# Kernel optimization log

Hardware: AMD Instinct MI355X
Metric: run time of the kernel (lower is better)

The kernel has to match this reference:

```python
import jax, jax.numpy as jnp
import numpy as np

EPS = 1e-12  # torch F.normalize default eps


def _l2norm(t, axis=-1):
    n = jnp.sqrt(jnp.sum(t * t, axis=axis, keepdims=True))
    return t / jnp.maximum(n, EPS)


def setup_inputs() -> dict:
    key = jax.random.key(0)
    ks = jax.random.split(key, 5)
    B, N, C, H = 8, 4096, 1024, 16
    x = jax.random.normal(ks[0], (B, N, C), dtype=jnp.float32)
    # nn.Linear(dim, 3*dim, bias=False): weight [3C, C]; we store transposed [C, 3C]
    w_qkv = jax.random.normal(ks[1], (C, 3 * C), dtype=jnp.float32) * (1.0 / np.sqrt(C))
    temperature = jnp.ones((H, 1, 1), dtype=jnp.float32)
    w_proj = jax.random.normal(ks[2], (C, C), dtype=jnp.float32) * (1.0 / np.sqrt(C))
    b_proj = jax.random.normal(ks[3], (C,), dtype=jnp.float32) * 0.01
    return {"x": x, "w_qkv": w_qkv, "temperature": temperature,
            "w_proj": w_proj, "b_proj": b_proj}


def reference(x, w_qkv, temperature, w_proj, b_proj):
    B, N, C = x.shape
    H = temperature.shape[0]
    dh = C // H
    # qkv: [B, N, 3C] -> [B, N, 3, H, dh] -> q/k/v each [B, H, dh, N]
    qkv = (x @ w_qkv).reshape(B, N, 3, H, dh).transpose(2, 0, 3, 4, 1)
    q, k, v = qkv[0], qkv[1], qkv[2]
    # L2-normalize over token axis (last dim)
    q = _l2norm(q)
    k = _l2norm(k)
    # channel-channel attention: [B, H, dh, dh]
    attn = jnp.einsum("bhdn,bhen->bhde", q, k) * temperature  # temp broadcasts [H,1,1]
    attn = jax.nn.softmax(attn, axis=-1)
    # weighted sum over channels: [B, H, dh, N] -> [B, N, C]
    out = jnp.einsum("bhde,bhen->bhdn", attn, v).transpose(0, 3, 1, 2).reshape(B, N, C)
    return out @ w_proj + b_proj
```

## Files before the change

kernel.cpp:

```cpp
#include <hip/hip_runtime.h>
#include <cstdint>

typedef unsigned short u16;
typedef unsigned int u32;
typedef __attribute__((ext_vector_type(8))) short bf16x8;
typedef __attribute__((ext_vector_type(4))) float f32x4;

typedef const u32 __attribute__((address_space(1)))* gp_t;
typedef u32 __attribute__((address_space(3)))* lp_t;

__device__ __forceinline__ u16 f2bf(float f) {
    union { float f; u32 u; } v; v.f = f;
    u32 r = v.u + 0x7FFFu + ((v.u >> 16) & 1u);
    return (u16)(r >> 16);
}
__device__ __forceinline__ float bf2f(u16 h) {
    union { u32 u; float f; } v; v.u = ((u32)h) << 16;
    return v.f;
}

__global__ __launch_bounds__(256) void k_pack2(const float* __restrict__ x,
                                               u16* __restrict__ xt, u16* __restrict__ xc) {
    __shared__ u16 tb[64][72];
    const int blk = blockIdx.x;
    const int tt = blk >> 4, ct = blk & 15;
    const long tok0 = (long)tt * 64;
    const int ch0 = ct * 64;
    const int tid = threadIdx.x;
    const int row = tid >> 2, cq = tid & 3;
#pragma unroll
    for (int jj = 0; jj < 4; ++jj) {
        const float4 v = *(const float4*)(x + (tok0 + row) * 1024 + ch0 + cq * 16 + jj * 4);
        tb[row][cq * 16 + jj * 4 + 0] = f2bf(v.x);
        tb[row][cq * 16 + jj * 4 + 1] = f2bf(v.y);
        tb[row][cq * 16 + jj * 4 + 2] = f2bf(v.z);
        tb[row][cq * 16 + jj * 4 + 3] = f2bf(v.w);
    }
    __syncthreads();
#pragma unroll
    for (int s = 0; s < 2; ++s) {
        const int c = s * 256 + tid;
        const int r2 = c >> 3, col8 = c & 7;
        *(uint4*)(xt + (tok0 + r2) * 1024 + ch0 + col8 * 8) = *(const uint4*)(&tb[r2][col8 * 8]);
    }
    const int b = (int)(tok0 >> 12);
    const int nin = (int)(tok0 & 4095);
#pragma unroll
    for (int s = 0; s < 2; ++s) {
        const int c = s * 256 + tid;
        const int crow = c >> 3, t8 = c & 7;
        u16 u[8];
#pragma unroll
        for (int k = 0; k < 8; ++k) u[k] = tb[t8 * 8 + k][crow];
        *(uint4*)(xc + ((long)b * 1024 + ch0 + crow) * 4096 + nin + t8 * 8) = *(const uint4*)u;
    }
}

__global__ void k_transpose_w(const float* __restrict__ src, u16* __restrict__ dst, int ncols) {
    __shared__ float t[64][65];
    int ntn = ncols >> 6;
    int kb = (blockIdx.x / ntn) * 64;
    int nb = (blockIdx.x % ntn) * 64;
    for (int i = threadIdx.x; i < 4096; i += 256) {
        int r = i >> 6, c = i & 63;
        t[r][c] = src[(long)(kb + r) * ncols + nb + c];
    }
    __syncthreads();
    for (int i = threadIdx.x; i < 4096; i += 256) {
        int r = i >> 6, c = i & 63;
        dst[(long)(nb + r) * 1024 + kb + c] = f2bf(t[c][r]);
    }
}

__global__ __launch_bounds__(256) void k_pack_wv(const float* __restrict__ wqkv, u16* __restrict__ wvb) {
    const int idx = blockIdx.x * 256 + threadIdx.x;
    const int cin = idx >> 7, e0 = (idx & 127) * 8;
    const float4 v1 = *(const float4*)(wqkv + (long)cin * 3072 + 2048 + e0);
    const float4 v2 = *(const float4*)(wqkv + (long)cin * 3072 + 2048 + e0 + 4);
    u16 u[8];
    u[0] = f2bf(v1.x); u[1] = f2bf(v1.y); u[2] = f2bf(v1.z); u[3] = f2bf(v1.w);
    u[4] = f2bf(v2.x); u[5] = f2bf(v2.y); u[6] = f2bf(v2.z); u[7] = f2bf(v2.w);
    *(uint4*)(wvb + (long)cin * 1024 + e0) = *(const uint4*)u;
}

__global__ __launch_bounds__(256) void k_g128p(
    const u16* __restrict__ xc, float* __restrict__ Sp)
{
    __shared__ u16 sm[8192];

    const int tid = threadIdx.x;
    const int wid = tid >> 6, lane = tid & 63;
    const int wr = wid >> 1, wc = wid & 1;
    const int fr = lane & 15, sl = lane >> 4;

    const int nwg = gridDim.x;
    const int logical = (blockIdx.x & 7) * (nwg >> 3) + (blockIdx.x >> 3);
    const int kseg = logical & 3;
    const int bt = logical >> 2;
    const int b = bt / 36;
    int t = bt % 36;
    int i0 = 0;
    while (t >= 8 - i0) { t -= 8 - i0; ++i0; }
    const int j0 = i0 + t;
    const int m0 = i0 * 128, n0 = j0 * 128;

    const u16* base = xc + (long)b * 4194304 + kseg * 1024;

    const int srow = lane >> 2;
    const int sslot = lane & 3;

    f32x4 acc[4][4];
#pragma unroll
    for (int i = 0; i < 4; ++i)
#pragma unroll
        for (int j = 0; j < 4; ++j) acc[i][j] = (f32x4){0.f, 0.f, 0.f, 0.f};

    for (int kt = 0; kt < 1024; kt += 32) {
        __syncthreads();
#pragma unroll
        for (int i = 0; i < 2; ++i) {
            const int row = wid * 32 + i * 16 + srow;
            const int swz = (sslot ^ ((row >> 1) & 3)) << 3;
            const u16* ga = base + (long)(m0 + row) * 4096 + kt + swz;
            const u16* gb = base + (long)(n0 + row) * 4096 + kt + swz;
            __builtin_amdgcn_global_load_lds((gp_t)ga, (lp_t)(sm + (wid * 2 + i) * 512), 16, 0, 0);
            __builtin_amdgcn_global_load_lds((gp_t)gb, (lp_t)(sm + 4096 + (wid * 2 + i) * 512), 16, 0, 0);
        }
        __syncthreads();
        bf16x8 af[4], bfr[4];
#pragma unroll
        for (int mi = 0; mi < 4; ++mi) {
            const int row = wr * 64 + mi * 16 + fr;
            af[mi] = *(const bf16x8*)(sm + row * 32 + ((sl ^ ((row >> 1) & 3)) << 3));
        }
#pragma unroll
        for (int ni = 0; ni < 4; ++ni) {
            const int row = wc * 64 + ni * 16 + fr;
            bfr[ni] = *(const bf16x8*)(sm + 4096 + row * 32 + ((sl ^ ((row >> 1) & 3)) << 3));
        }
#pragma unroll
        for (int mi = 0; mi < 4; ++mi)
#pragma unroll
            for (int ni = 0; ni < 4; ++ni)
                acc[mi][ni] = __builtin_amdgcn_mfma_f32_16x16x32_bf16(af[mi], bfr[ni], acc[mi][ni], 0, 0, 0);
    }

    float* gp = Sp + (long)logical * 16384;
#pragma unroll
    for (int mi = 0; mi < 4; ++mi)
#pragma unroll
        for (int ni = 0; ni < 4; ++ni)
#pragma unroll
            for (int rr = 0; rr < 4; ++rr)
                gp[(wr * 64 + mi * 16 + sl * 4 + rr) * 128 + wc * 64 + ni * 16 + fr] = acc[mi][ni][rr];
}

__global__ __launch_bounds__(256) void k_sred(const float* __restrict__ Sp, u16* __restrict__ S)
{
    __shared__ u16 lC[128 * 136];
    __shared__ u16 lCT[128 * 136];

    const int tid = threadIdx.x;
    const int nwg = gridDim.x;
    const int logical = (blockIdx.x & 7) * (nwg >> 3) + (blockIdx.x >> 3);
    const int b = logical / 36;
    int t = logical % 36;
    int i0 = 0;
    while (t >= 8 - i0) { t -= 8 - i0; ++i0; }
    const int j0 = i0 + t;
    const int m0 = i0 * 128, n0 = j0 * 128;

    const float* p = Sp + (long)logical * 65536;
    for (int i = tid; i < 16384; i += 256) {
        const float s = p[i] + p[i + 16384] + p[i + 32768] + p[i + 49152];
        const u16 v = f2bf(s);
        const int r_ = i >> 7, c_ = i & 127;
        lC[r_ * 136 + c_] = v;
        lCT[c_ * 136 + r_] = v;
    }
    __syncthreads();
    const int tk = tid >> 1, half = tid & 1;
    {
        u16* dp = S + (long)b * 1048576 + (long)(m0 + tk) * 1024 + n0 + half * 64;
        const u16* sp1 = lC + tk * 136 + half * 64;
#pragma unroll
        for (int i = 0; i < 8; ++i) ((uint4*)dp)[i] = ((const uint4*)sp1)[i];
    }
    if (i0 != j0) {
        u16* dp = S + (long)b * 1048576 + (long)(n0 + tk) * 1024 + m0 + half * 64;
        const u16* sp2 = lCT + tk * 136 + half * 64;
#pragma unroll
        for (int i = 0; i < 8; ++i) ((uint4*)dp)[i] = ((const uint4*)sp2)[i];
    }
}

__global__ __launch_bounds__(256) void k_g128(
    const u16* __restrict__ A, long Ab, const u16* __restrict__ Bt, long Bs,
    u16* __restrict__ C, long Cb, int K, int MT, int NT)
{
    __shared__ u16 sm[8192];
    __shared__ u16 lC[128 * 136];

    const int tid = threadIdx.x;
    const int wid = tid >> 6, lane = tid & 63;
    const int wr = wid >> 1, wc = wid & 1;
    const int fr = lane & 15, sl = lane >> 4;

    const int nwg = gridDim.x;
    const int logical = (blockIdx.x & 7) * (nwg >> 3) + (blockIdx.x >> 3);

    const int b = logical / (MT * NT);
    const int r = logical % (MT * NT);
    const int i0 = r / NT, j0 = r % NT;
    const int m0 = i0 * 128, n0 = j0 * 128;
    const u16* Abp = A + (long)b * Ab;
    const u16* Bbp = Bt + (long)b * Bs;
    u16* Cbp = C + (long)b * Cb;

    const int srow = lane >> 2;
    const int sslot = lane & 3;

    f32x4 acc[4][4];
#pragma unroll
    for (int i = 0; i < 4; ++i)
#pragma unroll
        for (int j = 0; j < 4; ++j) acc[i][j] = (f32x4){0.f, 0.f, 0.f, 0.f};

    for (int kt = 0; kt < K; kt += 32) {
        __syncthreads();
#pragma unroll
        for (int i = 0; i < 2; ++i) {
            const int row = wid * 32 + i * 16 + srow;
            const int swz = (sslot ^ ((row >> 1) & 3)) << 3;
            const u16* ga = Abp + (long)(m0 + row) * K + kt + swz;
            const u16* gb = Bbp + (long)(n0 + row) * K + kt + swz;
            __builtin_amdgcn_global_load_lds((gp_t)ga, (lp_t)(sm + (wid * 2 + i) * 512), 16, 0, 0);
            __builtin_amdgcn_global_load_lds((gp_t)gb, (lp_t)(sm + 4096 + (wid * 2 + i) * 512), 16, 0, 0);
        }
        __syncthreads();
        bf16x8 af[4], bfr[4];
#pragma unroll
        for (int mi = 0; mi < 4; ++mi) {
            const int row = wr * 64 + mi * 16 + fr;
            af[mi] = *(const bf16x8*)(sm + row * 32 + ((sl ^ ((row >> 1) & 3)) << 3));
        }
#pragma unroll
        for (int ni = 0; ni < 4; ++ni) {
            const int row = wc * 64 + ni * 16 + fr;
            bfr[ni] = *(const bf16x8*)(sm + 4096 + row * 32 + ((sl ^ ((row >> 1) & 3)) << 3));
        }
#pragma unroll
        for (int mi = 0; mi < 4; ++mi)
#pragma unroll
            for (int ni = 0; ni < 4; ++ni)
                acc[mi][ni] = __builtin_amdgcn_mfma_f32_16x16x32_bf16(af[mi], bfr[ni], acc[mi][ni], 0, 0, 0);
    }
    __syncthreads();

#pragma unroll
    for (int mi = 0; mi < 4; ++mi)
#pragma unroll
        for (int ni = 0; ni < 4; ++ni) {
            const int ch = wc * 64 + ni * 16 + fr;
            const int tk = wr * 64 + mi * 16 + sl * 4;
#pragma unroll
            for (int rr = 0; rr < 4; ++rr)
                lC[(tk + rr) * 136 + ch] = f2bf(acc[mi][ni][rr]);
        }
    __syncthreads();
    {
        const int tk = tid >> 1, half = tid & 1;
        const u16* sp = lC + tk * 136 + half * 64;
        u16* dp = Cbp + (long)(m0 + tk) * 1024 + n0 + half * 64;
#pragma unroll
        for (int i = 0; i < 8; ++i) ((uint4*)dp)[i] = ((const uint4*)sp)[i];
    }
}

template<int EPI>
__global__ __launch_bounds__(512, 2) void k_gemm256(
    const u16* __restrict__ A, long Ab, const u16* __restrict__ Bt, long Bs,
    int MT, int NT,
    u16* __restrict__ cB, float* __restrict__ cF, long Cb, const float* __restrict__ bias)
{
    __shared__ uint4 smem4[8704];
    u16* sm = (u16*)smem4;

    const int tid = threadIdx.x;
    const int wid = tid >> 6, lane = tid & 63;
    const int wr = wid >> 2, wc = wid & 3;
    const int fr = lane & 15, sl = lane >> 4;

    const int nwg = gridDim.x;
    const int logical = (blockIdx.x & 7) * (nwg >> 3) + (blockIdx.x >> 3);
    const int b = logical / (MT * NT);
    const int rem = logical % (MT * NT);
    const int mt = rem / NT, nt = rem % NT;
    const long m0 = (long)mt * 256;
    const int n0 = nt * 256;

    const int srow = wid * 32 + (lane >> 2);
    const int kswz = (((lane & 3) ^ ((srow >> 1) & 3)) << 3);
    const u16* gA = A + (long)b * Ab + (m0 + srow) * 1024L + kswz;
    const u16* gB = Bt + (long)b * Bs + ((long)n0 + srow) * 1024L + kswz;
    const int ldst = wid * 1024;

    const int fxor = ((sl ^ ((fr >> 1) & 3)) << 3);
    const int aBase = (wr * 128 + fr) * 32 + fxor;
    const int bBase = 32768 + (wc * 64 + fr) * 32 + fxor;

    f32x4 acc[8][4];
#pragma unroll
    for (int i = 0; i < 8; ++i)
#pragma unroll
        for (int j = 0; j < 4; ++j) acc[i][j] = (f32x4){0.f, 0.f, 0.f, 0.f};

#define STAGE_A(d, kh, ts) do { \
    const u16* g_ = gA + (ts) * 64 + (kh) * 32; \
    u16* l_ = sm + (d) * 16384 + (kh) * 8192 + ldst; \
    __builtin_amdgcn_global_load_lds((gp_t)g_, (lp_t)l_, 16, 0, 0); \
    __builtin_amdgcn_global_load_lds((gp_t)(g_ + 16 * 1024), (lp_t)(l_ + 512), 16, 0, 0); \
} while (0)
#define STAGE_B(d, kh, ts) do { \
    const u16* g_ = gB + (ts) * 64 + (kh) * 32; \
    u16* l_ = sm + 32768 + (d) * 16384 + (kh) * 8192 + ldst; \
    __builtin_amdgcn_global_load_lds((gp_t)g_, (lp_t)l_, 16, 0, 0); \
    __builtin_amdgcn_global_load_lds((gp_t)(g_ + 16 * 1024), (lp_t)(l_ + 512), 16, 0, 0); \
} while (0)

    STAGE_A(0, 0, 0); STAGE_B(0, 0, 0);
    STAGE_A(0, 1, 0); STAGE_B(0, 1, 0);
    STAGE_A(1, 0, 1); STAGE_B(1, 0, 1);
    asm volatile("s_waitcnt vmcnt(8)" ::: "memory");
    __builtin_amdgcn_s_barrier();

    bf16x8 afX[4], afY[4], bfX[4], bfY[4];
#pragma unroll
    for (int ni = 0; ni < 4; ++ni) bfX[ni] = *(const bf16x8*)(sm + bBase + ni * 512);
#pragma unroll
    for (int mi = 0; mi < 4; ++mi) afX[mi] = *(const bf16x8*)(sm + aBase + mi * 512);

#pragma unroll 2
    for (int T = 0; T < 16; ++T) {
        const int d = T & 1;
        const int t1 = (T + 1 < 16) ? T + 1 : 15;
        const int t2 = (T + 2 < 16) ? T + 2 : 15;
        const int base = d * 16384;
        const int nbase = (d ^ 1) * 16384;

#pragma unroll
        for (int mi = 0; mi < 4; ++mi)
            afY[mi] = *(const bf16x8*)(sm + aBase + (4 + mi) * 512 + base);
        STAGE_A(d ^ 1, 1, t1);
        asm volatile("s_waitcnt vmcnt(6)" ::: "memory");
        __builtin_amdgcn_s_barrier();
        __builtin_amdgcn_s_setprio(1);
#pragma unroll
        for (int mi = 0; mi < 4; ++mi)
#pragma unroll
            for (int ni = 0; ni < 4; ++ni)
                acc[mi][ni] = __builtin_amdgcn_mfma_f32_16x16x32_bf16(afX[mi], bfX[ni], acc[mi][ni], 0, 0, 0);
        __builtin_amdgcn_s_setprio(0);
        __builtin_amdgcn_s_barrier();

#pragma unroll
        for (int ni = 0; ni < 4; ++ni)
            bfY[ni] = *(const bf16x8*)(sm + bBase + ni * 512 + base + 8192);
#pragma unroll
        for (int mi = 0; mi < 4; ++mi)
            afX[mi] = *(const bf16x8*)(sm + aBase + mi * 512 + base + 8192);
        STAGE_B(d ^ 1, 1, t1);
        __builtin_amdgcn_s_barrier();
        __builtin_amdgcn_s_setprio(1);
#pragma unroll
        for (int mi = 0; mi < 4; ++mi)
#pragma unroll
            for (int ni = 0; ni < 4; ++ni)
                acc[mi + 4][ni] = __builtin_amdgcn_mfma_f32_16x16x32_bf16(afY[mi], bfX[ni], acc[mi + 4][ni], 0, 0, 0);
        __builtin_amdgcn_s_setprio(0);
        __builtin_amdgcn_s_barrier();

#pragma unroll
        for (int mi = 0; mi < 4; ++mi)
            afY[mi] = *(const bf16x8*)(sm + aBase + (4 + mi) * 512 + base + 8192);
        STAGE_A(d, 0, t2);
        asm volatile("s_waitcnt vmcnt(6)" ::: "memory");
        __builtin_amdgcn_s_barrier();
        __builtin_amdgcn_s_setprio(1);
#pragma unroll
        for (int mi = 0; mi < 4; ++mi)
#pragma unroll
            for (int ni = 0; ni < 4; ++ni)
                acc[mi][ni] = __builtin_amdgcn_mfma_f32_16x16x32_bf16(afX[mi], bfY[ni], acc[mi][ni], 0, 0, 0);
        __builtin_amdgcn_s_setprio(0);
        __builtin_amdgcn_s_barrier();

#pragma unroll
        for (int ni = 0; ni < 4; ++ni)
            bfX[ni] = *(const bf16x8*)(sm + bBase + ni * 512 + nbase);
#pragma unroll
        for (int mi = 0; mi < 4; ++mi)
            afX[mi] = *(const bf16x8*)(sm + aBase + mi * 512 + nbase);
        STAGE_B(d, 0, t2);
        __builtin_amdgcn_s_barrier();
        __builtin_amdgcn_s_setprio(1);
#pragma unroll
        for (int mi = 0; mi < 4; ++mi)
#pragma unroll
            for (int ni = 0; ni < 4; ++ni)
                acc[mi + 4][ni] = __builtin_amdgcn_mfma_f32_16x16x32_bf16(afY[mi], bfY[ni], acc[mi + 4][ni], 0, 0, 0);
        __builtin_amdgcn_s_setprio(0);
        __builtin_amdgcn_s_barrier();
    }
#undef STAGE_A
#undef STAGE_B
    asm volatile("s_waitcnt vmcnt(0)" ::: "memory");
    __syncthreads();

    if (EPI == 0) {
        u16* cbase = cB + (long)b * Cb;
        u16* piece = sm + wid * 8704;
#pragma unroll
        for (int mi = 0; mi < 8; ++mi)
#pragma unroll
            for (int ni = 0; ni < 4; ++ni) {
                const int ch = ni * 16 + fr;
                const int tk = mi * 16 + sl * 4;
#pragma unroll
                for (int rr = 0; rr < 4; ++rr)
                    piece[(tk + rr) * 68 + ch] = f2bf(acc[mi][ni][rr]);
            }
        __syncthreads();
#pragma unroll
        for (int i = 0; i < 32; ++i) {
            const int chunk = i * 512 + tid;
            const int row = chunk >> 4, c8 = chunk & 15;
            const int p = row >> 7, tk = row & 127;
            const int wrp = p >> 2, wcp = p & 3;
            const uint2 v = *(const uint2*)(sm + p * 8704 + tk * 68 + c8 * 4);
            *(uint2*)(cbase + (m0 + wrp * 128 + tk) * 1024L + n0 + wcp * 64 + c8 * 4) = v;
        }
    } else {
        float* cbase = cF + (long)b * Cb;
        float bi[4];
#pragma unroll
        for (int ni = 0; ni < 4; ++ni) bi[ni] = bias[n0 + wc * 64 + ni * 16 + fr];
#pragma unroll
        for (int pass = 0; pass < 2; ++pass) {
            float* pieceF = (float*)smem4 + wid * 4352;
            if (pass) __syncthreads();
#pragma unroll
            for (int mi2 = 0; mi2 < 4; ++mi2) {
                const int mi = pass * 4 + mi2;
#pragma unroll
                for (int ni = 0; ni < 4; ++ni) {
                    const int ch = ni * 16 + fr;
                    const int tk = mi2 * 16 + sl * 4;
#pragma unroll
                    for (int rr = 0; rr < 4; ++rr)
                        pieceF[(tk + rr) * 68 + ch] = acc[mi][ni][rr] + bi[ni];
                }
            }
            __syncthreads();
#pragma unroll
            for (int i = 0; i < 16; ++i) {
                const int chunk = i * 512 + tid;
                const int row = chunk >> 4, c4 = chunk & 15;
                const int p = row >> 6, tk = row & 63;
                const int wrp = p >> 2, wcp = p & 3;
                const float4 v = *(const float4*)((float*)smem4 + p * 4352 + tk * 68 + c4 * 4);
                *(float4*)(cbase + (m0 + wrp * 128 + pass * 64 + tk) * 1024L + n0 + wcp * 64 + c4 * 4) = v;
            }
        }
    }
}

__global__ __launch_bounds__(256) void k_gram2p(
    const u16* __restrict__ wqT, const u16* __restrict__ Ut,
    float* __restrict__ g2p, float* __restrict__ sq2p)
{
    __shared__ u16 lQ[64 * 256];
    __shared__ u16 lK[64 * 256];

    const int blk = blockIdx.x;
    const int seg = blk & 3, bh = blk >> 2;
    const int b = bh >> 4, h = bh & 15;
    const int tid = threadIdx.x;
    const int wid = tid >> 6, lane = tid & 63;

    {
        const int r2 = lane >> 5, slot = lane & 31;
        const int rbase = wid * 16;
#pragma unroll
        for (int i = 0; i < 8; ++i) {
            const int r = rbase + i * 2 + r2;
            const int col = seg * 256 + ((slot ^ (r & 7)) << 3);
            const u16* gq = wqT + (long)(h * 64 + r) * 1024 + col;
            const u16* gk = Ut + ((long)b * 2048 + 1024 + h * 64 + r) * 1024 + col;
            __builtin_amdgcn_global_load_lds((gp_t)gq, (lp_t)(lQ + (rbase + i * 2) * 256), 16, 0, 0);
            __builtin_amdgcn_global_load_lds((gp_t)gk, (lp_t)(lK + (rbase + i * 2) * 256), 16, 0, 0);
        }
    }
    __syncthreads();

    {
        const int row = tid >> 1, half = tid & 1;
        const int j = (row < 64) ? (h * 64 + row) : (1024 + h * 64 + (row - 64));
        const u16* pa = wqT + (long)j * 1024 + seg * 256 + half * 128;
        const u16* pb = Ut + ((long)b * 2048 + j) * 1024 + seg * 256 + half * 128;
        float s = 0.f;
#pragma unroll 4
        for (int i = 0; i < 16; ++i) {
            const uint4 a = *(const uint4*)(pa + i * 8);
            const uint4 bv = *(const uint4*)(pb + i * 8);
            s += bf2f((u16)(a.x & 0xFFFF)) * bf2f((u16)(bv.x & 0xFFFF));
            s += bf2f((u16)(a.x >> 16))    * bf2f((u16)(bv.x >> 16));
            s += bf2f((u16)(a.y & 0xFFFF)) * bf2f((u16)(bv.y & 0xFFFF));
            s += bf2f((u16)(a.y >> 16))    * bf2f((u16)(bv.y >> 16));
            s += bf2f((u16)(a.z & 0xFFFF)) * bf2f((u16)(bv.z & 0xFFFF));
            s += bf2f((u16)(a.z >> 16))    * bf2f((u16)(bv.z >> 16));
            s += bf2f((u16)(a.w & 0xFFFF)) * bf2f((u16)(bv.w & 0xFFFF));
            s += bf2f((u16)(a.w >> 16))    * bf2f((u16)(bv.w >> 16));
        }
        s += __shfl_xor(s, 1);
        if (half == 0) sq2p[(long)blk * 128 + row] = s;
    }

    const int fr = lane & 15, sl = lane >> 4;
    f32x4 acc[4];
#pragma unroll
    for (int i = 0; i < 4; ++i) acc[i] = (f32x4){0.f, 0.f, 0.f, 0.f};
#pragma unroll
    for (int ks = 0; ks < 8; ++ks) {
        const int ra = wid * 16 + fr;
        const bf16x8 a = *(const bf16x8*)(lQ + ra * 256 + (((ks * 4 + sl) ^ (ra & 7)) << 3));
#pragma unroll
        for (int ni = 0; ni < 4; ++ni) {
            const int rb = ni * 16 + fr;
            const bf16x8 bb = *(const bf16x8*)(lK + rb * 256 + (((ks * 4 + sl) ^ (rb & 7)) << 3));
            acc[ni] = __builtin_amdgcn_mfma_f32_16x16x32_bf16(a, bb, acc[ni], 0, 0, 0);
        }
    }
    float* gp = g2p + (long)blk * 4096;
#pragma unroll
    for (int ni = 0; ni < 4; ++ni)
#pragma unroll
        for (int rr = 0; rr < 4; ++rr)
            gp[(wid * 16 + sl * 4 + rr) * 64 + ni * 16 + fr] = acc[ni][rr];
}

__global__ __launch_bounds__(256) void k_smax2(
    const float* __restrict__ g2p, const float* __restrict__ sq2p,
    const float* __restrict__ temperature, u16* __restrict__ attn_g)
{
    const int row = blockIdx.x * 4 + (threadIdx.x >> 6);
    const int e = threadIdx.x & 63;
    const int bh = row >> 6, d = row & 63;
    const int h = bh & 15;
    float raw = 0.f, sqq = 0.f, sqk = 0.f;
    const float* gp = g2p + (long)bh * 16384 + d * 64 + e;
    const float* sp = sq2p + (long)bh * 512;
#pragma unroll
    for (int s = 0; s < 4; ++s) {
        raw += gp[s * 4096];
        sqq += sp[s * 128 + d];
        sqk += sp[s * 128 + 64 + e];
    }
    const float rq = 1.f / fmaxf(sqrtf(sqq), 1e-12f);
    const float rk = 1.f / fmaxf(sqrtf(sqk), 1e-12f);
    const float v = raw * rq * rk * temperature[h];
    float mx = v;
#pragma unroll
    for (int o = 32; o; o >>= 1) mx = fmaxf(mx, __shfl_xor(mx, o));
    const float p = __expf(v - mx);
    float sum = p;
#pragma unroll
    for (int o = 32; o; o >>= 1) sum += __shfl_xor(sum, o);
    attn_g[(long)row * 64 + e] = f2bf(p / sum);
}

__global__ __launch_bounds__(256) void k_wmix(
    const u16* __restrict__ attn_g, const u16* __restrict__ wpT, u16* __restrict__ wmix)
{
    __shared__ u16 lA[64 * 72];
    __shared__ u16 lB[256 * 64];

    const int blk = blockIdx.x;
    const int nseg = blk & 3, bh = blk >> 2;
    const int b = bh >> 4, h = bh & 15;
    const int tid = threadIdx.x;
    const int wid = tid >> 6, lane = tid & 63;
    const int fr = lane & 15, sl = lane >> 4;

#pragma unroll
    for (int i = 0; i < 8; ++i) {
        const int cc = wid * 8 + i;
        const int row = cc * 8 + (lane >> 3);
        const int slot = lane & 7;
        const u16* g = wpT + (long)(nseg * 256 + row) * 1024 + h * 64 + ((slot ^ (row & 7)) << 3);
        __builtin_amdgcn_global_load_lds((gp_t)g, (lp_t)(lB + cc * 512), 16, 0, 0);
    }
    {
        const u16* src = attn_g + (long)bh * 4096;
        for (int i = tid; i < 4096; i += 256) {
            const int d = i >> 6, e = i & 63;
            lA[e * 72 + d] = src[i];
        }
    }
    __syncthreads();

    f32x4 acc[4][4];
#pragma unroll
    for (int i = 0; i < 4; ++i)
#pragma unroll
        for (int j = 0; j < 4; ++j) acc[i][j] = (f32x4){0.f, 0.f, 0.f, 0.f};

#pragma unroll
    for (int ks = 0; ks < 2; ++ks) {
        bf16x8 a[4], bb[4];
#pragma unroll
        for (int mi = 0; mi < 4; ++mi)
            a[mi] = *(const bf16x8*)(lA + (mi * 16 + fr) * 72 + ks * 32 + sl * 8);
#pragma unroll
        for (int ni = 0; ni < 4; ++ni) {
            const int rb = wid * 64 + ni * 16 + fr;
            bb[ni] = *(const bf16x8*)(lB + rb * 64 + (((ks * 4 + sl) ^ (rb & 7)) << 3));
        }
#pragma unroll
        for (int mi = 0; mi < 4; ++mi)
#pragma unroll
            for (int ni = 0; ni < 4; ++ni)
                acc[mi][ni] = __builtin_amdgcn_mfma_f32_16x16x32_bf16(a[mi], bb[ni], acc[mi][ni], 0, 0, 0);
    }

    u16* dst = wmix + ((long)b << 20);
#pragma unroll
    for (int mi = 0; mi < 4; ++mi)
#pragma unroll
        for (int ni = 0; ni < 4; ++ni) {
            const int cout = nseg * 256 + wid * 64 + ni * 16 + fr;
            const int e0 = mi * 16 + sl * 4;
            ushort4 w;
            w.x = f2bf(acc[mi][ni][0]); w.y = f2bf(acc[mi][ni][1]);
            w.z = f2bf(acc[mi][ni][2]); w.w = f2bf(acc[mi][ni][3]);
            *(ushort4*)(dst + (long)cout * 1024 + h * 64 + e0) = w;
        }
}

extern "C" void kernel_launch(void* const* d_in, const int* in_sizes, int n_in,
                              void* d_out, int out_size, void* d_ws, size_t ws_size,
                              hipStream_t stream) {
    const float* x = (const float*)d_in[0];
    const float* w_qkv = (const float*)d_in[1];
    const float* temperature = (const float*)d_in[2];
    const float* w_proj = (const float*)d_in[3];
    const float* b_proj = (const float*)d_in[4];
    float* out = (float*)d_out;
    char* ws = (char*)d_ws;

    u16* wqT    = (u16*)(ws);
    u16* wpT    = (u16*)(ws + 6291456);
    u16* wvb    = (u16*)(ws + 8388608);
    u16* xt     = (u16*)(ws + 10485760);
    u16* xc     = (u16*)(ws + 77594624);
    u16* S      = (u16*)(ws + 144703488);
    float* Sp   = (float*)(ws + 161480704);
    u16* Ut     = (u16*)(ws + 161480704);
    float* g2p  = (float*)(ws + 195035136);
    float* sq2p = (float*)(ws + 203423744);
    u16* attn_g = (u16*)(ws + 203685888);
    u16* wmix   = (u16*)(ws + 204734464);
    u16* wfinT  = (u16*)(ws + 221511680);

    k_pack2<<<8192, 256, 0, stream>>>(x, xt, xc);
    k_transpose_w<<<768, 256, 0, stream>>>(w_qkv, wqT, 3072);
    k_transpose_w<<<256, 256, 0, stream>>>(w_proj, wpT, 1024);
    k_pack_wv<<<512, 256, 0, stream>>>(w_qkv, wvb);
    k_g128p<<<1152, 256, 0, stream>>>(xc, Sp);
    k_sred<<<288, 256, 0, stream>>>(Sp, S);
    k_gemm256<0><<<256, 512, 0, stream>>>(wqT, 0L, S, 1048576L, 8, 4, Ut, nullptr, 2097152L, nullptr);
    k_gram2p<<<512, 256, 0, stream>>>(wqT, Ut, g2p, sq2p);
    k_smax2<<<2048, 256, 0, stream>>>(g2p, sq2p, temperature, attn_g);
    k_wmix<<<512, 256, 0, stream>>>(attn_g, wpT, wmix);
    k_g128<<<512, 256, 0, stream>>>(wmix, 1048576L, wvb, 0L, wfinT, 1048576L, 1024, 8, 8);
    k_gemm256<1><<<512, 512, 0, stream>>>(xt, 4194304L, wfinT, 1048576L, 16, 4, nullptr, out, 4194304L, b_proj);
}
```

Before: 345.6 us.

## Merge weight prep kernels, fuse softmax into wmix, replace 256-tile GEMMs with 128-tile

Three weight-preparation kernels become one launch, and the softmax kernel is folded into the attention-weight mixing kernel so the bf16 attention matrix never round-trips through global memory. The heavily pipelined 256x256 GEMM kernel is removed. Its two uses now go to the simpler single-buffered 128x128 GEMM kernels, including a new float-output variant with a bias epilogue. This cuts launches and intermediate traffic, but gives up the deep double-buffered, priority-scheduled main loop in the largest GEMM, which may lower MFMA throughput.

```diff
diff --git a/kernel.cpp b/kernel.cpp
--- a/kernel.cpp
+++ b/kernel.cpp
@@ -56,31 +56,39 @@
     }
 }
 
-__global__ void k_transpose_w(const float* __restrict__ src, u16* __restrict__ dst, int ncols) {
+__global__ __launch_bounds__(256) void k_prep(
+    const float* __restrict__ wqkv, const float* __restrict__ wproj,
+    u16* __restrict__ wqT, u16* __restrict__ wpT, u16* __restrict__ wvb)
+{
     __shared__ float t[64][65];
-    int ntn = ncols >> 6;
-    int kb = (blockIdx.x / ntn) * 64;
-    int nb = (blockIdx.x % ntn) * 64;
-    for (int i = threadIdx.x; i < 4096; i += 256) {
-        int r = i >> 6, c = i & 63;
-        t[r][c] = src[(long)(kb + r) * ncols + nb + c];
-    }
-    __syncthreads();
-    for (int i = threadIdx.x; i < 4096; i += 256) {
-        int r = i >> 6, c = i & 63;
-        dst[(long)(nb + r) * 1024 + kb + c] = f2bf(t[c][r]);
-    }
-}
-
-__global__ __launch_bounds__(256) void k_pack_wv(const float* __restrict__ wqkv, u16* __restrict__ wvb) {
-    const int idx = blockIdx.x * 256 + threadIdx.x;
-    const int cin = idx >> 7, e0 = (idx & 127) * 8;
-    const float4 v1 = *(const float4*)(wqkv + (long)cin * 3072 + 2048 + e0);
-    const float4 v2 = *(const float4*)(wqkv + (long)cin * 3072 + 2048 + e0 + 4);
-    u16 u[8];
-    u[0] = f2bf(v1.x); u[1] = f2bf(v1.y); u[2] = f2bf(v1.z); u[3] = f2bf(v1.w);
-    u[4] = f2bf(v2.x); u[5] = f2bf(v2.y); u[6] = f2bf(v2.z); u[7] = f2bf(v2.w);
-    *(uint4*)(wvb + (long)cin * 1024 + e0) = *(const uint4*)u;
+    const int blk = blockIdx.x;
+    const int tid = threadIdx.x;
+    if (blk < 1024) {
+        const float* src; u16* dst; int ncols, lb;
+        if (blk < 768) { src = wqkv; dst = wqT; ncols = 3072; lb = blk; }
+        else           { src = wproj; dst = wpT; ncols = 1024; lb = blk - 768; }
+        const int ntn = ncols >> 6;
+        const int kb = (lb / ntn) * 64;
+        const int nb = (lb % ntn) * 64;
+        for (int i = tid; i < 4096; i += 256) {
+            int r = i >> 6, c = i & 63;
+            t[r][c] = src[(long)(kb + r) * ncols + nb + c];
+        }
+        __syncthreads();
+        for (int i = tid; i < 4096; i += 256) {
+            int r = i >> 6, c = i & 63;
+            dst[(long)(nb + r) * 1024 + kb + c] = f2bf(t[c][r]);
+        }
+    } else {
+        const int idx = (blk - 1024) * 256 + tid;
+        const int cin = idx >> 7, e0 = (idx & 127) * 8;
+        const float4 v1 = *(const float4*)(wqkv + (long)cin * 3072 + 2048 + e0);
+        const float4 v2 = *(const float4*)(wqkv + (long)cin * 3072 + 2048 + e0 + 4);
+        u16 u[8];
+        u[0] = f2bf(v1.x); u[1] = f2bf(v1.y); u[2] = f2bf(v1.z); u[3] = f2bf(v1.w);
+        u[4] = f2bf(v2.x); u[5] = f2bf(v2.y); u[6] = f2bf(v2.z); u[7] = f2bf(v2.w);
+        *(uint4*)(wvb + (long)cin * 1024 + e0) = *(const uint4*)u;
+    }
 }
 
 __global__ __launch_bounds__(256) void k_g128p(
@@ -277,200 +285,95 @@
     }
 }
 
-template<int EPI>
-__global__ __launch_bounds__(512, 2) void k_gemm256(
+__global__ __launch_bounds__(256) void k_g128f(
     const u16* __restrict__ A, long Ab, const u16* __restrict__ Bt, long Bs,
-    int MT, int NT,
-    u16* __restrict__ cB, float* __restrict__ cF, long Cb, const float* __restrict__ bias)
-{
-    __shared__ uint4 smem4[8704];
-    u16* sm = (u16*)smem4;
+    float* __restrict__ C, long Cb, int K, int MT, int NT, const float* __restrict__ bias)
+{
+    __shared__ u16 sm[8192];
+    __shared__ float lCf[4 * 2176];
 
     const int tid = threadIdx.x;
     const int wid = tid >> 6, lane = tid & 63;
-    const int wr = wid >> 2, wc = wid & 3;
+    const int wr = wid >> 1, wc = wid & 1;
     const int fr = lane & 15, sl = lane >> 4;
 
     const int nwg = gridDim.x;
     const int logical = (blockIdx.x & 7) * (nwg >> 3) + (blockIdx.x >> 3);
+
     const int b = logical / (MT * NT);
-    const int rem = logical % (MT * NT);
-    const int mt = rem / NT, nt = rem % NT;
-    const long m0 = (long)mt * 256;
-    const int n0 = nt * 256;
-
-    const int srow = wid * 32 + (lane >> 2);
-    const int kswz = (((lane & 3) ^ ((srow >> 1) & 3)) << 3);
-    const u16* gA = A + (long)b * Ab + (m0 + srow) * 1024L + kswz;
-    const u16* gB = Bt + (long)b * Bs + ((long)n0 + srow) * 1024L + kswz;
-    const int ldst = wid * 1024;
-
-    const int fxor = ((sl ^ ((fr >> 1) & 3)) << 3);
-    const int aBase = (wr * 128 + fr) * 32 + fxor;
-    const int bBase = 32768 + (wc * 64 + fr) * 32 + fxor;
-
-    f32x4 acc[8][4];
-#pragma unroll
-    for (int i = 0; i < 8; ++i)
+    const int r = logical % (MT * NT);
+    const int i0 = r / NT, j0 = r % NT;
+    const int m0 = i0 * 128, n0 = j0 * 128;
+    const u16* Abp = A + (long)b * Ab;
+    const u16* Bbp = Bt + (long)b * Bs;
+    float* Cbp = C + (long)b * Cb;
+
+    const int srow = lane >> 2;
+    const int sslot = lane & 3;
+
+    f32x4 acc[4][4];
+#pragma unroll
+    for (int i = 0; i < 4; ++i)
 #pragma unroll
         for (int j = 0; j < 4; ++j) acc[i][j] = (f32x4){0.f, 0.f, 0.f, 0.f};
 
-#define STAGE_A(d, kh, ts) do { \
-    const u16* g_ = gA + (ts) * 64 + (kh) * 32; \
-    u16* l_ = sm + (d) * 16384 + (kh) * 8192 + ldst; \
-    __builtin_amdgcn_global_load_lds((gp_t)g_, (lp_t)l_, 16, 0, 0); \
-    __builtin_amdgcn_global_load_lds((gp_t)(g_ + 16 * 1024), (lp_t)(l_ + 512), 16, 0, 0); \
-} while (0)
-#define STAGE_B(d, kh, ts) do { \
-    const u16* g_ = gB + (ts) * 64 + (kh) * 32; \
-    u16* l_ = sm + 32768 + (d) * 16384 + (kh) * 8192 + ldst; \
-    __builtin_amdgcn_global_load_lds((gp_t)g_, (lp_t)l_, 16, 0, 0); \
-    __builtin_amdgcn_global_load_lds((gp_t)(g_ + 16 * 1024), (lp_t)(l_ + 512), 16, 0, 0); \
-} while (0)
-
-    STAGE_A(0, 0, 0); STAGE_B(0, 0, 0);
-    STAGE_A(0, 1, 0); STAGE_B(0, 1, 0);
-    STAGE_A(1, 0, 1); STAGE_B(1, 0, 1);
-    asm volatile("s_waitcnt vmcnt(8)" ::: "memory");
-    __builtin_amdgcn_s_barrier();
-
-    bf16x8 afX[4], afY[4], bfX[4], bfY[4];
-#pragma unroll
-    for (int ni = 0; ni < 4; ++ni) bfX[ni] = *(const bf16x8*)(sm + bBase + ni * 512);
-#pragma unroll
-    for (int mi = 0; mi < 4; ++mi) afX[mi] = *(const bf16x8*)(sm + aBase + mi * 512);
-
-#pragma unroll 2
-    for (int T = 0; T < 16; ++T) {
-        const int d = T & 1;
-        const int t1 = (T + 1 < 16) ? T + 1 : 15;
-        const int t2 = (T + 2 < 16) ? T + 2 : 15;
-        const int base = d * 16384;
-        const int nbase = (d ^ 1) * 16384;
-
+    for (int kt = 0; kt < K; kt += 32) {
+        __syncthreads();
+#pragma unroll
+        for (int i = 0; i < 2; ++i) {
+            const int row = wid * 32 + i * 16 + srow;
+            const int swz = (sslot ^ ((row >> 1) & 3)) << 3;
+            const u16* ga = Abp + (long)(m0 + row) * K + kt + swz;
+            const u16* gb = Bbp + (long)(n0 + row) * K + kt + swz;
+            __builtin_amdgcn_global_load_lds((gp_t)ga, (lp_t)(sm + (wid * 2 + i) * 512), 16, 0, 0);
+            __builtin_amdgcn_global_load_lds((gp_t)gb, (lp_t)(sm + 4096 + (wid * 2 + i) * 512), 16, 0, 0);
+        }
+        __syncthreads();
+        bf16x8 af[4], bfr[4];
+#pragma unroll
+        for (int mi = 0; mi < 4; ++mi) {
+            const int row = wr * 64 + mi * 16 + fr;
+            af[mi] = *(const bf16x8*)(sm + row * 32 + ((sl ^ ((row >> 1) & 3)) << 3));
+        }
+#pragma unroll
+        for (int ni = 0; ni < 4; ++ni) {
+            const int row = wc * 64 + ni * 16 + fr;
+            bfr[ni] = *(const bf16x8*)(sm + 4096 + row * 32 + ((sl ^ ((row >> 1) & 3)) << 3));
+        }
 #pragma unroll
         for (int mi = 0; mi < 4; ++mi)
-            afY[mi] = *(const bf16x8*)(sm + aBase + (4 + mi) * 512 + base);
-        STAGE_A(d ^ 1, 1, t1);
-        asm volatile("s_waitcnt vmcnt(6)" ::: "memory");
-        __builtin_amdgcn_s_barrier();
-        __builtin_amdgcn_s_setprio(1);
-#pragma unroll
-        for (int mi = 0; mi < 4; ++mi)
 #pragma unroll
             for (int ni = 0; ni < 4; ++ni)
-                acc[mi][ni] = __builtin_amdgcn_mfma_f32_16x16x32_bf16(afX[mi], bfX[ni], acc[mi][ni], 0, 0, 0);
-        __builtin_amdgcn_s_setprio(0);
-        __builtin_amdgcn_s_barrier();
-
-#pragma unroll
-        for (int ni = 0; ni < 4; ++ni)
-            bfY[ni] = *(const bf16x8*)(sm + bBase + ni * 512 + base + 8192);
-#pragma unroll
-        for (int mi = 0; mi < 4; ++mi)
-            afX[mi] = *(const bf16x8*)(sm + aBase + mi * 512 + base + 8192);
-        STAGE_B(d ^ 1, 1, t1);
-        __builtin_amdgcn_s_barrier();
-        __builtin_amdgcn_s_setprio(1);
-#pragma unroll
-        for (int mi = 0; mi < 4; ++mi)
+                acc[mi][ni] = __builtin_amdgcn_mfma_f32_16x16x32_bf16(af[mi], bfr[ni], acc[mi][ni], 0, 0, 0);
+    }
+    __syncthreads();
+
+    float bi[4];
+#pragma unroll
+    for (int ni = 0; ni < 4; ++ni) bi[ni] = bias[n0 + wc * 64 + ni * 16 + fr];
+
+#pragma unroll
+    for (int pass = 0; pass < 2; ++pass) {
+        if (pass) __syncthreads();
+        float* piece = lCf + (wr * 2 + wc) * 2176;
+#pragma unroll
+        for (int mi2 = 0; mi2 < 2; ++mi2) {
+            const int mi = pass * 2 + mi2;
 #pragma unroll
             for (int ni = 0; ni < 4; ++ni)
-                acc[mi + 4][ni] = __builtin_amdgcn_mfma_f32_16x16x32_bf16(afY[mi], bfX[ni], acc[mi + 4][ni], 0, 0, 0);
-        __builtin_amdgcn_s_setprio(0);
-        __builtin_amdgcn_s_barrier();
-
-#pragma unroll
-        for (int mi = 0; mi < 4; ++mi)
-            afY[mi] = *(const bf16x8*)(sm + aBase + (4 + mi) * 512 + base + 8192);
-        STAGE_A(d, 0, t2);
-        asm volatile("s_waitcnt vmcnt(6)" ::: "memory");
-        __builtin_amdgcn_s_barrier();
-        __builtin_amdgcn_s_setprio(1);
-#pragma unroll
-        for (int mi = 0; mi < 4; ++mi)
-#pragma unroll
-            for (int ni = 0; ni < 4; ++ni)
-                acc[mi][ni] = __builtin_amdgcn_mfma_f32_16x16x32_bf16(afX[mi], bfY[ni], acc[mi][ni], 0, 0, 0);
-        __builtin_amdgcn_s_setprio(0);
-        __builtin_amdgcn_s_barrier();
-
-#pragma unroll
-        for (int ni = 0; ni < 4; ++ni)
-            bfX[ni] = *(const bf16x8*)(sm + bBase + ni * 512 + nbase);
-#pragma unroll
-        for (int mi = 0; mi < 4; ++mi)
-            afX[mi] = *(const bf16x8*)(sm + aBase + mi * 512 + nbase);
-        STAGE_B(d, 0, t2);
-        __builtin_amdgcn_s_barrier();
-        __builtin_amdgcn_s_setprio(1);
-#pragma unroll
-        for (int mi = 0; mi < 4; ++mi)
-#pragma unroll
-            for (int ni = 0; ni < 4; ++ni)
-                acc[mi + 4][ni] = __builtin_amdgcn_mfma_f32_16x16x32_bf16(afY[mi], bfY[ni], acc[mi + 4][ni], 0, 0, 0);
-        __builtin_amdgcn_s_setprio(0);
-        __builtin_amdgcn_s_barrier();
-    }
-#undef STAGE_A
-#undef STAGE_B
-    asm volatile("s_waitcnt vmcnt(0)" ::: "memory");
-    __syncthreads();
-
-    if (EPI == 0) {
-        u16* cbase = cB + (long)b * Cb;
-        u16* piece = sm + wid * 8704;
-#pragma unroll
-        for (int mi = 0; mi < 8; ++mi)
-#pragma unroll
-            for (int ni = 0; ni < 4; ++ni) {
-                const int ch = ni * 16 + fr;
-                const int tk = mi * 16 + sl * 4;
 #pragma unroll
                 for (int rr = 0; rr < 4; ++rr)
-                    piece[(tk + rr) * 68 + ch] = f2bf(acc[mi][ni][rr]);
-            }
-        __syncthreads();
-#pragma unroll
-        for (int i = 0; i < 32; ++i) {
-            const int chunk = i * 512 + tid;
-            const int row = chunk >> 4, c8 = chunk & 15;
-            const int p = row >> 7, tk = row & 127;
-            const int wrp = p >> 2, wcp = p & 3;
-            const uint2 v = *(const uint2*)(sm + p * 8704 + tk * 68 + c8 * 4);
-            *(uint2*)(cbase + (m0 + wrp * 128 + tk) * 1024L + n0 + wcp * 64 + c8 * 4) = v;
-        }
-    } else {
-        float* cbase = cF + (long)b * Cb;
-        float bi[4];
-#pragma unroll
-        for (int ni = 0; ni < 4; ++ni) bi[ni] = bias[n0 + wc * 64 + ni * 16 + fr];
-#pragma unroll
-        for (int pass = 0; pass < 2; ++pass) {
-            float* pieceF = (float*)smem4 + wid * 4352;
-            if (pass) __syncthreads();
-#pragma unroll
-            for (int mi2 = 0; mi2 < 4; ++mi2) {
-                const int mi = pass * 4 + mi2;
-#pragma unroll
-                for (int ni = 0; ni < 4; ++ni) {
-                    const int ch = ni * 16 + fr;
-                    const int tk = mi2 * 16 + sl * 4;
-#pragma unroll
-                    for (int rr = 0; rr < 4; ++rr)
-                        pieceF[(tk + rr) * 68 + ch] = acc[mi][ni][rr] + bi[ni];
-                }
-            }
-            __syncthreads();
-#pragma unroll
-            for (int i = 0; i < 16; ++i) {
-                const int chunk = i * 512 + tid;
-                const int row = chunk >> 4, c4 = chunk & 15;
-                const int p = row >> 6, tk = row & 63;
-                const int wrp = p >> 2, wcp = p & 3;
-                const float4 v = *(const float4*)((float*)smem4 + p * 4352 + tk * 68 + c4 * 4);
-                *(float4*)(cbase + (m0 + wrp * 128 + pass * 64 + tk) * 1024L + n0 + wcp * 64 + c4 * 4) = v;
-            }
+                    piece[(mi2 * 16 + sl * 4 + rr) * 68 + ni * 16 + fr] = acc[mi][ni][rr] + bi[ni];
+        }
+        __syncthreads();
+#pragma unroll
+        for (int i = 0; i < 8; ++i) {
+            const int chunk = i * 256 + tid;
+            const int lr = chunk >> 5, c4 = chunk & 31;
+            const int wrp = lr >> 5, r32 = lr & 31;
+            const int wcp = c4 >> 4;
+            const float4 v = *(const float4*)(lCf + (wrp * 2 + wcp) * 2176 + r32 * 68 + (c4 & 15) * 4);
+            *(float4*)(Cbp + (long)(m0 + wrp * 64 + pass * 32 + r32) * 1024 + n0 + wcp * 64 + (c4 & 15) * 4) = v;
         }
     }
 }
@@ -549,38 +452,10 @@
             gp[(wid * 16 + sl * 4 + rr) * 64 + ni * 16 + fr] = acc[ni][rr];
 }
 
-__global__ __launch_bounds__(256) void k_smax2(
+__global__ __launch_bounds__(256) void k_swmix(
     const float* __restrict__ g2p, const float* __restrict__ sq2p,
-    const float* __restrict__ temperature, u16* __restrict__ attn_g)
-{
-    const int row = blockIdx.x * 4 + (threadIdx.x >> 6);
-    const int e = threadIdx.x & 63;
-    const int bh = row >> 6, d = row & 63;
-    const int h = bh & 15;
-    float raw = 0.f, sqq = 0.f, sqk = 0.f;
-    const float* gp = g2p + (long)bh * 16384 + d * 64 + e;
-    const float* sp = sq2p + (long)bh * 512;
-#pragma unroll
-    for (int s = 0; s < 4; ++s) {
-        raw += gp[s * 4096];
-        sqq += sp[s * 128 + d];
-        sqk += sp[s * 128 + 64 + e];
-    }
-    const float rq = 1.f / fmaxf(sqrtf(sqq), 1e-12f);
-    const float rk = 1.f / fmaxf(sqrtf(sqk), 1e-12f);
-    const float v = raw * rq * rk * temperature[h];
-    float mx = v;
-#pragma unroll
-    for (int o = 32; o; o >>= 1) mx = fmaxf(mx, __shfl_xor(mx, o));
-    const float p = __expf(v - mx);
-    float sum = p;
-#pragma unroll
-    for (int o = 32; o; o >>= 1) sum += __shfl_xor(sum, o);
-    attn_g[(long)row * 64 + e] = f2bf(p / sum);
-}
-
-__global__ __launch_bounds__(256) void k_wmix(
-    const u16* __restrict__ attn_g, const u16* __restrict__ wpT, u16* __restrict__ wmix)
+    const float* __restrict__ temperature,
+    const u16* __restrict__ wpT, u16* __restrict__ wmix)
 {
     __shared__ u16 lA[64 * 72];
     __shared__ u16 lB[256 * 64];
@@ -600,11 +475,35 @@
         const u16* g = wpT + (long)(nseg * 256 + row) * 1024 + h * 64 + ((slot ^ (row & 7)) << 3);
         __builtin_amdgcn_global_load_lds((gp_t)g, (lp_t)(lB + cc * 512), 16, 0, 0);
     }
+
     {
-        const u16* src = attn_g + (long)bh * 4096;
-        for (int i = tid; i < 4096; i += 256) {
-            const int d = i >> 6, e = i & 63;
-            lA[e * 72 + d] = src[i];
+        const int e = lane;
+        const float* sp = sq2p + (long)bh * 512;
+        float sqk = 0.f;
+#pragma unroll
+        for (int s = 0; s < 4; ++s) sqk += sp[s * 128 + 64 + e];
+        const float rk = 1.f / fmaxf(sqrtf(sqk), 1e-12f);
+        const float temp = temperature[h];
+        const float* gp = g2p + (long)bh * 16384;
+#pragma unroll 2
+        for (int i = 0; i < 16; ++i) {
+            const int d = wid * 16 + i;
+            float raw = 0.f, sqq = 0.f;
+#pragma unroll
+            for (int s = 0; s < 4; ++s) {
+                raw += gp[s * 4096 + d * 64 + e];
+                sqq += sp[s * 128 + d];
+            }
+            const float rq = 1.f / fmaxf(sqrtf(sqq), 1e-12f);
+            const float v = raw * rq * rk * temp;
+            float mx = v;
+#pragma unroll
+            for (int o = 32; o; o >>= 1) mx = fmaxf(mx, __shfl_xor(mx, o));
+            const float p = __expf(v - mx);
+            float sum = p;
+#pragma unroll
+            for (int o = 32; o; o >>= 1) sum += __shfl_xor(sum, o);
+            lA[e * 72 + d] = f2bf(p / sum);
         }
     }
     __syncthreads();
@@ -668,20 +567,16 @@
     u16* Ut     = (u16*)(ws + 161480704);
     float* g2p  = (float*)(ws + 195035136);
     float* sq2p = (float*)(ws + 203423744);
-    u16* attn_g = (u16*)(ws + 203685888);
     u16* wmix   = (u16*)(ws + 204734464);
     u16* wfinT  = (u16*)(ws + 221511680);
 
     k_pack2<<<8192, 256, 0, stream>>>(x, xt, xc);
-    k_transpose_w<<<768, 256, 0, stream>>>(w_qkv, wqT, 3072);
-    k_transpose_w<<<256, 256, 0, stream>>>(w_proj, wpT, 1024);
-    k_pack_wv<<<512, 256, 0, stream>>>(w_qkv, wvb);
+    k_prep<<<1536, 256, 0, stream>>>(w_qkv, w_proj, wqT, wpT, wvb);
     k_g128p<<<1152, 256, 0, stream>>>(xc, Sp);
     k_sred<<<288, 256, 0, stream>>>(Sp, S);
-    k_gemm256<0><<<256, 512, 0, stream>>>(wqT, 0L, S, 1048576L, 8, 4, Ut, nullptr, 2097152L, nullptr);
+    k_g128<<<1024, 256, 0, stream>>>(wqT, 0L, S, 1048576L, Ut, 2097152L, 1024, 16, 8);
     k_gram2p<<<512, 256, 0, stream>>>(wqT, Ut, g2p, sq2p);
-    k_smax2<<<2048, 256, 0, stream>>>(g2p, sq2p, temperature, attn_g);
-    k_wmix<<<512, 256, 0, stream>>>(attn_g, wpT, wmix);
+    k_swmix<<<512, 256, 0, stream>>>(g2p, sq2p, temperature, wpT, wmix);
     k_g128<<<512, 256, 0, stream>>>(wmix, 1048576L, wvb, 0L, wfinT, 1048576L, 1024, 8, 8);
-    k_gemm256<1><<<512, 512, 0, stream>>>(xt, 4194304L, wfinT, 1048576L, 16, 4, nullptr, out, 4194304L, b_proj);
-}
+    k_g128f<<<2048, 256, 0, stream>>>(xt, 4194304L, wfinT, 1048576L, out, 4194304L, 1024, 32, 8, b_proj);
+}
```

Measured after the change: 408.7 us. 18.3% more time.
